# Performance work log

Hardware: AMD Instinct MI355X
Metric: run time of the kernel (lower is better)

Reference implementation:

```python
import jax, jax.numpy as jnp
import numpy as np

HEADS = 16
DIM_HEAD = 64
DIM = 1024
LN_EPS = 1e-5


def _split_heads(x):
    # [b, n, h*d] -> [b, h, n, d]
    b, n, _ = x.shape
    return x.reshape(b, n, HEADS, DIM_HEAD).transpose(0, 2, 1, 3)


def _rmsnorm(x, gamma):
    # F.normalize over last dim, then * sqrt(dim_head) * gamma ([h,1,d])
    nrm = jnp.sqrt(jnp.sum(x * x, axis=-1, keepdims=True))
    normed = x / jnp.maximum(nrm, 1e-12)
    return normed * (DIM_HEAD ** 0.5) * gamma


def setup_inputs() -> dict:
    key = jax.random.key(0)
    ks = jax.random.split(key, 8)
    inner = HEADS * DIM_HEAD
    q = jax.random.normal(ks[0], (8, 128, DIM), dtype=jnp.float32)
    kv = jax.random.normal(ks[1], (8, 4096, DIM), dtype=jnp.float32)
    mask = jax.random.bernoulli(ks[2], 0.9, (8, 4096))  # bool, True = keep
    ln_w = jnp.ones((DIM,), dtype=jnp.float32)
    gamma_q = jnp.ones((HEADS, 1, DIM_HEAD), dtype=jnp.float32)
    gamma_k = jnp.ones((HEADS, 1, DIM_HEAD), dtype=jnp.float32)
    s = 1.0 / np.sqrt(DIM)
    Wq = jax.random.normal(ks[3], (DIM, inner), dtype=jnp.float32) * s
    Wkv = jax.random.normal(ks[4], (DIM, 2 * inner), dtype=jnp.float32) * s
    Wout = jax.random.normal(ks[5], (inner, DIM), dtype=jnp.float32) * (1.0 / np.sqrt(inner))
    return {"q": q, "kv": kv, "mask": mask, "ln_w": ln_w,
            "gamma_q": gamma_q, "gamma_k": gamma_k,
            "Wq": Wq, "Wkv": Wkv, "Wout": Wout}


def reference(q, kv, mask, ln_w, gamma_q, gamma_k, Wq, Wkv, Wout):
    # LayerNorm (no bias) on queries only
    mu = jnp.mean(q, axis=-1, keepdims=True)
    var = jnp.mean(jnp.square(q - mu), axis=-1, keepdims=True)
    qn = (q - mu) / jnp.sqrt(var + LN_EPS) * ln_w

    inner = HEADS * DIM_HEAD
    Q = qn @ Wq                      # [b, nq, inner]
    KVp = kv @ Wkv                   # [b, nkv, 2*inner]
    K, V = KVp[..., :inner], KVp[..., inner:]

    Qh = _rmsnorm(_split_heads(Q), gamma_q)   # [b, h, nq, d]
    Kh = _rmsnorm(_split_heads(K), gamma_k)   # [b, h, nkv, d]
    Vh = _split_heads(V)                      # [b, h, nkv, d]

    dots = jnp.einsum('bhnd,bhmd->bhnm', Qh, Kh)  # no 1/sqrt(d): scale lives in RMSNorm
    neg = -jnp.finfo(dots.dtype).max
    dots = jnp.where(mask[:, None, None, :], dots, neg)
    attn = jax.nn.softmax(dots, axis=-1)

    out = jnp.einsum('bhnm,bhmd->bhnd', attn, Vh)
    b, h, n, d = out.shape
    out = out.transpose(0, 2, 1, 3).reshape(b, n, h * d)
    return out @ Wout
```

## Files before the change

### kernel.cpp

```cpp
#include <hip/hip_runtime.h>
#include <cfloat>
#include <cstdint>


typedef _Float16 f16;
typedef _Float16 f16x8 __attribute__((ext_vector_type(8)));
typedef _Float16 f16x4 __attribute__((ext_vector_type(4)));
typedef float    f32x4 __attribute__((ext_vector_type(4)));

#define DEV __device__ __forceinline__

DEV f32x4 mfma16(f16x8 a, f16x8 b, f32x4 c) {
  return __builtin_amdgcn_mfma_f32_16x16x32_f16(a, b, c, 0, 0, 0);
}

DEV void gl_lds16(const void* g, void* l) {
  __builtin_amdgcn_global_load_lds(
      (const __attribute__((address_space(1))) uint32_t*)g,
      (__attribute__((address_space(3))) uint32_t*)l, 16, 0, 0);
}


__global__ __launch_bounds__(256) void cast_f16_kernel(
    const float* __restrict__ src, f16* __restrict__ dst, int n4) {
  int stride = gridDim.x * 256;
  for (int i = blockIdx.x * 256 + threadIdx.x; i < n4; i += stride) {
    float4 v = ((const float4*)src)[i];
    f16x4 o = { (f16)v.x, (f16)v.y, (f16)v.z, (f16)v.w };
    ((f16x4*)dst)[i] = o;
  }
}

__global__ __launch_bounds__(256) void transpose_cast_kernel(
    const float* __restrict__ src, f16* __restrict__ dst, int ldsrc, int lddst) {
  __shared__ float tile[32][33];
  int c0 = blockIdx.x * 32, r0 = blockIdx.y * 32;
  int tx = threadIdx.x & 31, ty = threadIdx.x >> 5;
  #pragma unroll
  for (int i = 0; i < 4; ++i)
    tile[ty + i * 8][tx] = src[(long)(r0 + ty + i * 8) * ldsrc + c0 + tx];
  __syncthreads();
  #pragma unroll
  for (int i = 0; i < 4; ++i)
    dst[(long)(c0 + ty + i * 8) * lddst + r0 + tx] = (f16)tile[tx][ty + i * 8];
}

__global__ __launch_bounds__(256) void ln_kernel(
    const float* __restrict__ q, const float* __restrict__ w, f16* __restrict__ qn) {
  int row = blockIdx.x, tid = threadIdx.x;
  float4 v = ((const float4*)(q + (long)row * 1024))[tid];
  float s1 = v.x + v.y + v.z + v.w;
  float s2 = v.x * v.x + v.y * v.y + v.z * v.z + v.w * v.w;
  #pragma unroll
  for (int off = 1; off < 64; off <<= 1) {
    s1 += __shfl_xor(s1, off);
    s2 += __shfl_xor(s2, off);
  }
  __shared__ float r1[4], r2[4];
  int wid = tid >> 6;
  if ((tid & 63) == 0) { r1[wid] = s1; r2[wid] = s2; }
  __syncthreads();
  s1 = r1[0] + r1[1] + r1[2] + r1[3];
  s2 = r2[0] + r2[1] + r2[2] + r2[3];
  float mu = s1 * (1.0f / 1024.0f);
  float var = s2 * (1.0f / 1024.0f) - mu * mu;
  float rstd = rsqrtf(var + 1e-5f);
  float4 wv = ((const float4*)w)[tid];
  f16x4 o = { (f16)((v.x - mu) * rstd * wv.x), (f16)((v.y - mu) * rstd * wv.y),
              (f16)((v.z - mu) * rstd * wv.z), (f16)((v.w - mu) * rstd * wv.w) };
  ((f16x4*)(qn + (long)row * 1024))[tid] = o;
}

template <int OUT_F16, int NORM>
__global__ __launch_bounds__(256) void gemm128(
    const f16* __restrict__ A, const f16* __restrict__ BT, void* __restrict__ C,
    const float* __restrict__ gamma,
    int M, int N, int K, int lda, int ldb, int ldc) {
  __shared__ f16 tA[128 * 32];
  __shared__ f16 tB[128 * 32];
  const int tid = threadIdx.x, lane = tid & 63, wid = tid >> 6;
  const int wr = wid >> 1, wc = wid & 1;
  const int c = lane & 15, g = lane >> 4;
  const int m0 = blockIdx.y * 128, n0 = blockIdx.x * 128;
  f32x4 acc[4][4] = {};
  for (int k0 = 0; k0 < K; k0 += 32) {
    __syncthreads();
    #pragma unroll
    for (int ii = 0; ii < 2; ++ii) {
      int i = tid + ii * 256;
      gl_lds16(A + (long)(m0 + (i >> 2)) * lda + k0 + (i & 3) * 8, tA + i * 8);
    }
    #pragma unroll
    for (int ii = 0; ii < 2; ++ii) {
      int i = tid + ii * 256;
      gl_lds16(BT + (long)(n0 + (i >> 2)) * ldb + k0 + (i & 3) * 8, tB + i * 8);
    }
    __syncthreads();
    f16x8 af[4], bfr[4];
    #pragma unroll
    for (int mi = 0; mi < 4; ++mi)
      af[mi] = *(const f16x8*)&tA[(wr * 64 + mi * 16 + c) * 32 + g * 8];
    #pragma unroll
    for (int ni = 0; ni < 4; ++ni)
      bfr[ni] = *(const f16x8*)&tB[(wc * 64 + ni * 16 + c) * 32 + g * 8];
    #pragma unroll
    for (int mi = 0; mi < 4; ++mi)
      #pragma unroll
      for (int ni = 0; ni < 4; ++ni)
        acc[mi][ni] = mfma16(af[mi], bfr[ni], acc[mi][ni]);
  }
  float gam[4];
  if (NORM) {
    #pragma unroll
    for (int ni = 0; ni < 4; ++ni) gam[ni] = gamma[n0 + wc * 64 + ni * 16 + c];
    #pragma unroll
    for (int mi = 0; mi < 4; ++mi)
      #pragma unroll
      for (int j = 0; j < 4; ++j) {
        float s = 0.f;
        #pragma unroll
        for (int ni = 0; ni < 4; ++ni) { float x = acc[mi][ni][j]; s += x * x; }
        s += __shfl_xor(s, 1); s += __shfl_xor(s, 2);
        s += __shfl_xor(s, 4); s += __shfl_xor(s, 8);
        float sc = 8.0f / fmaxf(sqrtf(s), 1e-12f);
        #pragma unroll
        for (int ni = 0; ni < 4; ++ni) acc[mi][ni][j] *= sc * gam[ni];
      }
  }
  #pragma unroll
  for (int mi = 0; mi < 4; ++mi)
    #pragma unroll
    for (int ni = 0; ni < 4; ++ni)
      #pragma unroll
      for (int j = 0; j < 4; ++j) {
        int row = m0 + wr * 64 + mi * 16 + g * 4 + j;
        int col = n0 + wc * 64 + ni * 16 + c;
        if (OUT_F16) ((f16*)C)[(long)row * ldc + col] = (f16)acc[mi][ni][j];
        else        ((float*)C)[(long)row * ldc + col] = acc[mi][ni][j];
      }
}

__global__ __launch_bounds__(512, 2) void gemm256(
    const f16* __restrict__ A, const f16* __restrict__ BT, f16* __restrict__ C,
    const float* __restrict__ gamma, int normLim,
    int K, int lda, int ldb, int ldc, int mtiles, int ntiles) {
  __shared__ f16 lds[4 * 16384];
  const int tid = threadIdx.x, lane = tid & 63, wid = tid >> 6;
  const int wr = wid >> 2, wc = wid & 3;
  const int c = lane & 15, g = lane >> 4;
  const int nwg = mtiles * ntiles, cpx = nwg >> 3;
  const int bid = blockIdx.x;
  const int wg = (bid & 7) * cpx + (bid >> 3);
  const int n0 = (wg % ntiles) * 256;
  const long m0 = (long)(wg / ntiles) * 256;

  const int nkt = K >> 5;
  const int r1 = tid >> 2, r2 = 128 + (tid >> 2), sl = tid & 3;
  const int sw1 = (sl ^ (r1 & 3)) << 3, sw2 = (sl ^ (r2 & 3)) << 3;

  f32x4 acc[8][4] = {};

  #define STAGE_A(kt_) do { int kt__ = (kt_);                                   \
    f16* dst = lds + ((kt__) & 3) * 16384; int k0 = (kt__) << 5;                \
    gl_lds16(A + (m0 + r1) * lda + k0 + sw1, dst + (long)tid * 8);              \
    gl_lds16(A + (m0 + r2) * lda + k0 + sw2, dst + (long)(tid + 512) * 8);      \
  } while (0)
  #define STAGE_B(kt_) do { int kt__ = (kt_);                                   \
    f16* dst = lds + ((kt__) & 3) * 16384 + 8192; int k0 = (kt__) << 5;         \
    gl_lds16(BT + (long)(n0 + r1) * ldb + k0 + sw1, dst + (long)tid * 8);       \
    gl_lds16(BT + (long)(n0 + r2) * ldb + k0 + sw2, dst + (long)(tid + 512) * 8);\
  } while (0)

  STAGE_A(0); STAGE_B(0); STAGE_A(1); STAGE_B(1);
  asm volatile("s_waitcnt vmcnt(4)" ::: "memory");
  __builtin_amdgcn_s_barrier();

  for (int kt = 0; kt < nkt; ++kt) {
    const f16* la = lds + (kt & 3) * 16384;
    const f16* lb = la + 8192;
    const bool pre = (kt + 2) < nkt;
    if (pre) STAGE_A(kt + 2);
    f16x8 bfr[4], afr[4];
    #pragma unroll
    for (int ni = 0; ni < 4; ++ni) {
      int r = wc * 64 + ni * 16 + c;
      bfr[ni] = *(const f16x8*)&lb[r * 32 + ((g ^ (r & 3)) << 3)];
    }
    #pragma unroll
    for (int q = 0; q < 4; ++q) {
      int r = wr * 128 + q * 16 + c;
      afr[q] = *(const f16x8*)&la[r * 32 + ((g ^ (r & 3)) << 3)];
    }
    __builtin_amdgcn_s_setprio(1);
    #pragma unroll
    for (int q = 0; q < 4; ++q)
      #pragma unroll
      for (int ni = 0; ni < 4; ++ni)
        acc[q][ni] = mfma16(afr[q], bfr[ni], acc[q][ni]);
    __builtin_amdgcn_s_setprio(0);
    if (pre) STAGE_B(kt + 2);
    #pragma unroll
    for (int q = 0; q < 4; ++q) {
      int r = wr * 128 + 64 + q * 16 + c;
      afr[q] = *(const f16x8*)&la[r * 32 + ((g ^ (r & 3)) << 3)];
    }
    __builtin_amdgcn_s_setprio(1);
    #pragma unroll
    for (int q = 0; q < 4; ++q)
      #pragma unroll
      for (int ni = 0; ni < 4; ++ni)
        acc[4 + q][ni] = mfma16(afr[q], bfr[ni], acc[4 + q][ni]);
    __builtin_amdgcn_s_setprio(0);
    if (pre) { asm volatile("s_waitcnt vmcnt(4)" ::: "memory"); }
    else     { asm volatile("s_waitcnt vmcnt(0)" ::: "memory"); }
    __builtin_amdgcn_s_barrier();
  }
  #undef STAGE_A
  #undef STAGE_B

  const int colbase = n0 + wc * 64;
  if (colbase < normLim) {
    float gam[4];
    #pragma unroll
    for (int ni = 0; ni < 4; ++ni) gam[ni] = gamma[colbase + ni * 16 + c];
    #pragma unroll
    for (int mi = 0; mi < 8; ++mi)
      #pragma unroll
      for (int j = 0; j < 4; ++j) {
        float s = 0.f;
        #pragma unroll
        for (int ni = 0; ni < 4; ++ni) { float x = acc[mi][ni][j]; s += x * x; }
        s += __shfl_xor(s, 1); s += __shfl_xor(s, 2);
        s += __shfl_xor(s, 4); s += __shfl_xor(s, 8);
        float sc = 8.0f / fmaxf(sqrtf(s), 1e-12f);
        #pragma unroll
        for (int ni = 0; ni < 4; ++ni) acc[mi][ni][j] *= sc * gam[ni];
      }
  }
  #pragma unroll
  for (int mi = 0; mi < 8; ++mi)
    #pragma unroll
    for (int j = 0; j < 4; ++j) {
      long row = m0 + wr * 128 + mi * 16 + g * 4 + j;
      #pragma unroll
      for (int ni = 0; ni < 4; ++ni)
        C[row * ldc + colbase + ni * 16 + c] = (f16)acc[mi][ni][j];
    }
}

__global__ __launch_bounds__(256) void attn_kernel(
    const f16* __restrict__ Q, const f16* __restrict__ KV,
    const int* __restrict__ mask, f16* __restrict__ O) {
  __shared__ f16 Kt[64 * 64];
  __shared__ f16 Vt[64 * 72];
  __shared__ f16 Pl[4 * 16 * 72];
  const int blk = blockIdx.x;
  const int half = blk & 1, h = (blk >> 1) & 15, b = blk >> 5;
  const int tid = threadIdx.x, lane = tid & 63, wid = tid >> 6;
  const int c = lane & 15, g = lane >> 4;

  const int qrow = b * 128 + half * 64 + wid * 16 + c;
  f16x8 qa[2];
  #pragma unroll
  for (int kk = 0; kk < 2; ++kk)
    qa[kk] = *(const f16x8*)&Q[(long)qrow * 1024 + h * 64 + kk * 32 + g * 8];

  float m_[4], l_[4];
  f32x4 o_[4];
  #pragma unroll
  for (int j = 0; j < 4; ++j) { m_[j] = -FLT_MAX; l_[j] = 0.f; }
  #pragma unroll
  for (int ni = 0; ni < 4; ++ni) o_[ni] = (f32x4){0.f, 0.f, 0.f, 0.f};

  const long kvbase = (long)b * 4096 * 2048;
  f16* Pw = Pl + wid * 16 * 72;

  for (int kt = 0; kt < 64; ++kt) {
    __syncthreads();
    #pragma unroll
    for (int ii = 0; ii < 2; ++ii) {
      int i = tid + ii * 256;
      int r = i >> 3, s = i & 7;
      gl_lds16(KV + kvbase + (long)(kt * 64 + r) * 2048 + h * 64 + ((s ^ (r & 7)) * 8),
               Kt + i * 8);
    }
    #pragma unroll
    for (int ii = 0; ii < 2; ++ii) {
      int i = tid + ii * 256;
      int kv = i & 63, d0 = (i >> 6) * 8;
      f16x8 v = *(const f16x8*)&KV[kvbase + (long)(kt * 64 + kv) * 2048 + 1024 + h * 64 + d0];
      #pragma unroll
      for (int j = 0; j < 8; ++j) Vt[(d0 + j) * 72 + kv] = v[j];
    }
    __syncthreads();

    f32x4 s4[4];
    #pragma unroll
    for (int ni = 0; ni < 4; ++ni) {
      s4[ni] = (f32x4){0.f, 0.f, 0.f, 0.f};
      int kvr = ni * 16 + c;
      #pragma unroll
      for (int kk = 0; kk < 2; ++kk) {
        int slot = (kk * 4 + g) ^ (kvr & 7);
        f16x8 kb = *(const f16x8*)&Kt[kvr * 64 + slot * 8];
        s4[ni] = mfma16(qa[kk], kb, s4[ni]);
      }
    }

    int msk[4];
    #pragma unroll
    for (int ni = 0; ni < 4; ++ni) {
      msk[ni] = mask[b * 4096 + kt * 64 + ni * 16 + c];
      if (!msk[ni]) s4[ni] = (f32x4){-FLT_MAX, -FLT_MAX, -FLT_MAX, -FLT_MAX};
    }

    float mnew[4], alpha[4], psum[4];
    #pragma unroll
    for (int j = 0; j < 4; ++j) {
      float v = fmaxf(fmaxf(s4[0][j], s4[1][j]), fmaxf(s4[2][j], s4[3][j]));
      v = fmaxf(v, __shfl_xor(v, 1));
      v = fmaxf(v, __shfl_xor(v, 2));
      v = fmaxf(v, __shfl_xor(v, 4));
      v = fmaxf(v, __shfl_xor(v, 8));
      mnew[j] = fmaxf(m_[j], v);
      alpha[j] = __expf(m_[j] - mnew[j]);
      m_[j] = mnew[j];
      psum[j] = 0.f;
    }
    f16 pb[4][4];
    #pragma unroll
    for (int ni = 0; ni < 4; ++ni)
      #pragma unroll
      for (int j = 0; j < 4; ++j) {
        float p = msk[ni] ? __expf(s4[ni][j] - mnew[j]) : 0.0f;
        psum[j] += p;
        pb[ni][j] = (f16)p;
      }
    #pragma unroll
    for (int j = 0; j < 4; ++j) {
      float ps = psum[j];
      ps += __shfl_xor(ps, 1);
      ps += __shfl_xor(ps, 2);
      ps += __shfl_xor(ps, 4);
      ps += __shfl_xor(ps, 8);
      l_[j] = alpha[j] * l_[j] + ps;
    }
    #pragma unroll
    for (int ni = 0; ni < 4; ++ni)
      #pragma unroll
      for (int j = 0; j < 4; ++j)
        Pw[(g * 4 + j) * 72 + ni * 16 + c] = pb[ni][j];
    #pragma unroll
    for (int ni = 0; ni < 4; ++ni)
      #pragma unroll
      for (int j = 0; j < 4; ++j)
        o_[ni][j] *= alpha[j];
    f16x8 pa[2];
    #pragma unroll
    for (int kk = 0; kk < 2; ++kk)
      pa[kk] = *(const f16x8*)&Pw[c * 72 + kk * 32 + g * 8];
    #pragma unroll
    for (int ni = 0; ni < 4; ++ni)
      #pragma unroll
      for (int kk = 0; kk < 2; ++kk) {
        f16x8 vb = *(const f16x8*)&Vt[(ni * 16 + c) * 72 + kk * 32 + g * 8];
        o_[ni] = mfma16(pa[kk], vb, o_[ni]);
      }
  }

  #pragma unroll
  for (int j = 0; j < 4; ++j) {
    float inv = 1.0f / fmaxf(l_[j], 1e-30f);
    int row = b * 128 + half * 64 + wid * 16 + g * 4 + j;
    #pragma unroll
    for (int ni = 0; ni < 4; ++ni) {
      int col = h * 64 + ni * 16 + c;
      O[(long)row * 1024 + col] = (f16)(o_[ni][j] * inv);
    }
  }
}


extern "C" void kernel_launch(void* const* d_in, const int* in_sizes, int n_in,
                              void* d_out, int out_size, void* d_ws, size_t ws_size,
                              hipStream_t stream) {
  const float* q    = (const float*)d_in[0];
  const float* kv   = (const float*)d_in[1];
  const int*   mask = (const int*)d_in[2];
  const float* ln_w = (const float*)d_in[3];
  const float* gq   = (const float*)d_in[4];
  const float* gk   = (const float*)d_in[5];
  const float* Wq   = (const float*)d_in[6];
  const float* Wkv  = (const float*)d_in[7];
  const float* Wout = (const float*)d_in[8];
  float* out = (float*)d_out;
  char* ws = (char*)d_ws;
  const size_t MB = (size_t)1 << 20;
  f16* qn    = (f16*)(ws + 0 * MB);
  f16* Qm    = (f16*)(ws + 2 * MB);
  f16* Om    = (f16*)(ws + 4 * MB);
  f16* WqT   = (f16*)(ws + 6 * MB);
  f16* WkvT  = (f16*)(ws + 8 * MB);
  f16* WoutT = (f16*)(ws + 12 * MB);
  f16* kv16  = (f16*)(ws + 14 * MB);
  f16* KVp   = (f16*)(ws + 78 * MB);

  cast_f16_kernel<<<2048, 256, 0, stream>>>(kv, kv16, 8 * 4096 * 1024 / 4);
  transpose_cast_kernel<<<dim3(32, 32), 256, 0, stream>>>(Wq, WqT, 1024, 1024);
  transpose_cast_kernel<<<dim3(64, 32), 256, 0, stream>>>(Wkv, WkvT, 2048, 1024);
  transpose_cast_kernel<<<dim3(32, 32), 256, 0, stream>>>(Wout, WoutT, 1024, 1024);
  ln_kernel<<<1024, 256, 0, stream>>>(q, ln_w, qn);
  gemm128<1, 1><<<dim3(8, 8), 256, 0, stream>>>(qn, WqT, Qm, gq,
                                                1024, 1024, 1024, 1024, 1024, 1024);
  gemm256<<<1024, 512, 0, stream>>>(kv16, WkvT, KVp, gk, 1024,
                                    1024, 1024, 1024, 2048, 128, 8);
  attn_kernel<<<256, 256, 0, stream>>>(Qm, KVp, mask, Om);
  gemm128<0, 0><<<dim3(8, 8), 256, 0, stream>>>(Om, WoutT, out, nullptr,
                                                1024, 1024, 1024, 1024, 1024, 1024);
}
```

Measured before the change: 569.2 us.

## Split attention over KV chunks with a merge kernel; change GEMM LDS swizzle

```diff
diff --git a/kernel.cpp b/kernel.cpp
--- a/kernel.cpp
+++ b/kernel.cpp
@@ -156,7 +156,7 @@
 
   const int nkt = K >> 5;
   const int r1 = tid >> 2, r2 = 128 + (tid >> 2), sl = tid & 3;
-  const int sw1 = (sl ^ (r1 & 3)) << 3, sw2 = (sl ^ (r2 & 3)) << 3;
+  const int sw1 = (sl ^ ((r1 >> 1) & 3)) << 3, sw2 = (sl ^ ((r2 >> 1) & 3)) << 3;
 
   f32x4 acc[8][4] = {};
 
@@ -184,12 +184,12 @@
     #pragma unroll
     for (int ni = 0; ni < 4; ++ni) {
       int r = wc * 64 + ni * 16 + c;
-      bfr[ni] = *(const f16x8*)&lb[r * 32 + ((g ^ (r & 3)) << 3)];
+      bfr[ni] = *(const f16x8*)&lb[r * 32 + ((g ^ ((r >> 1) & 3)) << 3)];
     }
     #pragma unroll
     for (int q = 0; q < 4; ++q) {
       int r = wr * 128 + q * 16 + c;
-      afr[q] = *(const f16x8*)&la[r * 32 + ((g ^ (r & 3)) << 3)];
+      afr[q] = *(const f16x8*)&la[r * 32 + ((g ^ ((r >> 1) & 3)) << 3)];
     }
     __builtin_amdgcn_s_setprio(1);
     #pragma unroll
@@ -202,7 +202,7 @@
     #pragma unroll
     for (int q = 0; q < 4; ++q) {
       int r = wr * 128 + 64 + q * 16 + c;
-      afr[q] = *(const f16x8*)&la[r * 32 + ((g ^ (r & 3)) << 3)];
+      afr[q] = *(const f16x8*)&la[r * 32 + ((g ^ ((r >> 1) & 3)) << 3)];
     }
     __builtin_amdgcn_s_setprio(1);
     #pragma unroll
@@ -250,12 +250,14 @@
 
 __global__ __launch_bounds__(256) void attn_kernel(
     const f16* __restrict__ Q, const f16* __restrict__ KV,
-    const int* __restrict__ mask, f16* __restrict__ O) {
+    const int* __restrict__ mask, float* __restrict__ Opart,
+    float* __restrict__ ml) {
   __shared__ f16 Kt[64 * 64];
   __shared__ f16 Vt[64 * 72];
   __shared__ f16 Pl[4 * 16 * 72];
   const int blk = blockIdx.x;
-  const int half = blk & 1, h = (blk >> 1) & 15, b = blk >> 5;
+  const int chunk = blk >> 8, sub = blk & 255;
+  const int half = sub & 1, h = (sub >> 1) & 15, b = sub >> 5;
   const int tid = threadIdx.x, lane = tid & 63, wid = tid >> 6;
   const int c = lane & 15, g = lane >> 4;
 
@@ -275,7 +277,7 @@
   const long kvbase = (long)b * 4096 * 2048;
   f16* Pw = Pl + wid * 16 * 72;
 
-  for (int kt = 0; kt < 64; ++kt) {
+  for (int kt = chunk * 16; kt < chunk * 16 + 16; ++kt) {
     __syncthreads();
     #pragma unroll
     for (int ii = 0; ii < 2; ++ii) {
@@ -370,14 +372,39 @@
 
   #pragma unroll
   for (int j = 0; j < 4; ++j) {
-    float inv = 1.0f / fmaxf(l_[j], 1e-30f);
     int row = b * 128 + half * 64 + wid * 16 + g * 4 + j;
     #pragma unroll
-    for (int ni = 0; ni < 4; ++ni) {
-      int col = h * 64 + ni * 16 + c;
-      O[(long)row * 1024 + col] = (f16)(o_[ni][j] * inv);
-    }
-  }
+    for (int ni = 0; ni < 4; ++ni)
+      Opart[((long)chunk * 1024 + row) * 1024 + h * 64 + ni * 16 + c] = o_[ni][j];
+    if (c == 0) {
+      long u = (((long)chunk * 1024 + row) * 16 + h) * 2;
+      ml[u] = m_[j];
+      ml[u + 1] = l_[j];
+    }
+  }
+}
+
+__global__ __launch_bounds__(256) void attn_merge_kernel(
+    const float* __restrict__ Opart, const float* __restrict__ ml,
+    f16* __restrict__ Om) {
+  int unit = blockIdx.x * 4 + (threadIdx.x >> 6);
+  int lane = threadIdx.x & 63;
+  int row = unit >> 4, h = unit & 15;
+  float mc[4], lc[4], M = -FLT_MAX;
+  #pragma unroll
+  for (int cI = 0; cI < 4; ++cI) {
+    long u = (((long)cI * 1024 + row) * 16 + h) * 2;
+    mc[cI] = ml[u]; lc[cI] = ml[u + 1];
+    M = fmaxf(M, mc[cI]);
+  }
+  float L = 0.f, o = 0.f;
+  #pragma unroll
+  for (int cI = 0; cI < 4; ++cI) {
+    float w = __expf(mc[cI] - M);
+    L += lc[cI] * w;
+    o += Opart[((long)cI * 1024 + row) * 1024 + h * 64 + lane] * w;
+  }
+  Om[(long)row * 1024 + h * 64 + lane] = (f16)(o / fmaxf(L, 1e-30f));
 }
 
 
@@ -403,6 +430,8 @@
   f16* WkvT  = (f16*)(ws + 8 * MB);
   f16* WoutT = (f16*)(ws + 12 * MB);
   f16* kv16  = (f16*)(ws + 14 * MB);
+  float* Opart = (float*)(ws + 14 * MB);
+  float* mlb   = (float*)(ws + 30 * MB);
   f16* KVp   = (f16*)(ws + 78 * MB);
 
   cast_f16_kernel<<<2048, 256, 0, stream>>>(kv, kv16, 8 * 4096 * 1024 / 4);
@@ -414,7 +443,8 @@
                                                 1024, 1024, 1024, 1024, 1024, 1024);
   gemm256<<<1024, 512, 0, stream>>>(kv16, WkvT, KVp, gk, 1024,
                                     1024, 1024, 1024, 2048, 128, 8);
-  attn_kernel<<<256, 256, 0, stream>>>(Qm, KVp, mask, Om);
+  attn_kernel<<<1024, 256, 0, stream>>>(Qm, KVp, mask, Opart, mlb);
+  attn_merge_kernel<<<4096, 256, 0, stream>>>(Opart, mlb, Om);
   gemm128<0, 0><<<dim3(8, 8), 256, 0, stream>>>(Om, WoutT, out, nullptr,
                                                 1024, 1024, 1024, 1024, 1024, 1024);
 }
```

Result: faster. 515.5 us (-9.4%).
